# Performance work log

Measured on AMD Instinct MI355X. Metric: run time of the kernel, lower is better.

Reference implementation:

```python
import math
import jax, jax.numpy as jnp
import numpy as np

C = 256
CQ = C // 8
B, H, W = 8, 64, 64


def setup_inputs() -> dict:
    key = jax.random.key(0)
    k1, k2, k3, k4 = jax.random.split(key, 4)
    x = jax.random.normal(k1, (B, C, H, W), dtype=jnp.float32)
    # 1x1 conv weights, bias=False -> plain [out, in] matrices
    wq = jax.random.normal(k2, (CQ, C), dtype=jnp.float32) * 0.02
    wk = jax.random.normal(k3, (CQ, C), dtype=jnp.float32) * 0.02
    wv = jax.random.normal(k4, (C, C), dtype=jnp.float32) * 0.02
    # gamma init is zeros in the torch module; use small nonzero so output depends on attention path
    gamma = jnp.ones((1,), dtype=jnp.float32) * 0.5
    return {"x": x, "wq": wq, "wk": wk, "wv": wv, "gamma": gamma}


def reference(x, wq, wk, wv, gamma):
    b, c, h, w = x.shape
    n = h * w
    xr = x.reshape(b, c, n)                       # [B, C, N]
    q = jnp.einsum('oc,bcn->bon', wq, xr)         # [B, Cq, N]
    k = jnp.einsum('oc,bcn->bon', wk, xr)         # [B, Cq, N]
    v = jnp.einsum('oc,bcn->bon', wv, xr)         # [B, C, N]
    # attn[b, i, j] = softmax_j( q[:, i] . k[:, j] / sqrt(Cq) )
    scores = jnp.einsum('bci,bcj->bij', q, k) / math.sqrt(q.shape[1])  # [B, N, N]
    attn = jax.nn.softmax(scores, axis=-1)
    # out[b, c, m] = sum_n v[b, c, n] * attn[b, m, n]
    out = jnp.einsum('bcn,bmn->bcm', v, attn).reshape(b, c, h, w)
    return gamma[0] * out + x
```

## Files before the change

### kernel.cpp

```cpp
#include <hip/hip_runtime.h>

#define B_ 8
#define C_ 256
#define CQ_ 32
#define N_ 4096

typedef __attribute__((ext_vector_type(8))) short short8;
typedef __attribute__((ext_vector_type(4))) float float4v;

#define QSCALE 0.2550599232f

#if __has_builtin(__builtin_amdgcn_exp2f)
#define EXP2F __builtin_amdgcn_exp2f
#else
#define EXP2F exp2f
#endif

static __device__ __forceinline__ unsigned short f2bf(float f) {
  unsigned int u = __float_as_uint(f);
  u += 0x7FFFu + ((u >> 16) & 1u);
  return (unsigned short)(u >> 16);
}

static __device__ __forceinline__ void async16(void* lds, const void* g) {
  __builtin_amdgcn_global_load_lds(
      (const __attribute__((address_space(1))) unsigned int*)g,
      (__attribute__((address_space(3))) unsigned int*)lds, 16, 0, 0);
}

__global__ __launch_bounds__(256) void conv_kernel(
    const float* __restrict__ x, const float* __restrict__ wq,
    const float* __restrict__ wk, const float* __restrict__ wv,
    unsigned short* __restrict__ xT, unsigned short* __restrict__ w_bf) {
  int tid = threadIdx.x, nt = blockIdx.x, b = blockIdx.y;
  if (nt == 64) {
    #pragma unroll 1
    for (int i = 0; i < 40; ++i) {
      int o = b * 40 + i;
      const float* src; float sc = 1.f;
      if (o < 32)      { src = wq + (size_t)o * 256; sc = QSCALE; }
      else if (o < 64) { src = wk + (size_t)(o - 32) * 256; }
      else             { src = wv + (size_t)(o - 64) * 256; }
      w_bf[o * 256 + tid] = f2bf(src[tid] * sc);
    }
    return;
  }
  __shared__ __align__(16) unsigned short t_lds[16 * 264];
  int n0 = nt * 64;
  const float* xp = x + ((size_t)b * C_ + tid) * N_ + n0;
  #pragma unroll 1
  for (int nl = 0; nl < 4; ++nl) {
    float4 f[4];
    #pragma unroll
    for (int i = 0; i < 4; ++i) f[i] = *(const float4*)(xp + nl * 16 + i * 4);
    if (nl) __syncthreads();
    #pragma unroll
    for (int i = 0; i < 4; ++i) {
      t_lds[(i * 4 + 0) * 264 + tid] = f2bf(f[i].x);
      t_lds[(i * 4 + 1) * 264 + tid] = f2bf(f[i].y);
      t_lds[(i * 4 + 2) * 264 + tid] = f2bf(f[i].z);
      t_lds[(i * 4 + 3) * 264 + tid] = f2bf(f[i].w);
    }
    __syncthreads();
    int row = tid >> 4, col = (tid & 15) * 16;
    uint4 a0 = *(const uint4*)(&t_lds[row * 264 + col]);
    uint4 a1 = *(const uint4*)(&t_lds[row * 264 + col + 8]);
    unsigned short* dst = xT + ((size_t)b * N_ + n0 + nl * 16 + row) * 256 + col;
    *(uint4*)(dst) = a0;
    *(uint4*)(dst + 8) = a1;
  }
}

__global__ __launch_bounds__(256, 2) void proj_kernel(
    const unsigned short* __restrict__ xT, const unsigned short* __restrict__ w_bf,
    unsigned short* __restrict__ qT, unsigned short* __restrict__ kT,
    unsigned short* __restrict__ v) {
  __shared__ __align__(16) unsigned short xb[2][256 * 32];
  int tid = threadIdx.x, wave = tid >> 6, lane = tid & 63;
  int q16 = lane >> 4, l16 = lane & 15;
  int b = blockIdx.x, n0 = blockIdx.y * 256, ot = blockIdx.z;

  short8 af[4][8];
  #pragma unroll
  for (int mt = 0; mt < 4; ++mt)
    #pragma unroll
    for (int ks = 0; ks < 8; ++ks)
      af[mt][ks] = *(const short8*)(w_bf + (size_t)(ot * 64 + mt * 16 + l16) * 256 + ks * 32 + q16 * 8);

  const unsigned short* xbase = xT + ((size_t)b * N_ + n0) * 256;
  auto stage = [&](int buf, int ks) {
    #pragma unroll
    for (int it = 0; it < 4; ++it) {
      int r = wave * 64 + it * 16 + (lane >> 2);
      int lo = (lane & 3) ^ ((r >> 1) & 3);
      async16(&xb[buf][(wave * 64 + it * 16) * 32],
              xbase + (size_t)r * 256 + ks * 32 + lo * 8);
    }
  };

  float4v acc[4][4];
  float4v zerov = {0.f, 0.f, 0.f, 0.f};
  #pragma unroll
  for (int mt = 0; mt < 4; ++mt)
    for (int nt = 0; nt < 4; ++nt) acc[mt][nt] = zerov;

  stage(0, 0);
  __syncthreads();

  int po = (( l16 >> 1) & 3);
  #pragma unroll
  for (int ks = 0; ks < 8; ++ks) {
    if (ks < 7) stage((ks + 1) & 1, ks + 1);
    short8 bf4[4];
    #pragma unroll
    for (int nt = 0; nt < 4; ++nt) {
      int row = wave * 64 + nt * 16 + l16;
      bf4[nt] = *(const short8*)(&xb[ks & 1][row * 32 + (q16 ^ po) * 8]);
    }
    #pragma unroll
    for (int mt = 0; mt < 4; ++mt)
      #pragma unroll
      for (int nt = 0; nt < 4; ++nt)
        acc[mt][nt] = __builtin_amdgcn_mfma_f32_16x16x32_bf16(af[mt][ks], bf4[nt], acc[mt][nt], 0, 0, 0);
    __syncthreads();
  }

  #pragma unroll
  for (int mt = 0; mt < 4; ++mt) {
    int og0 = ot * 64 + mt * 16;
    #pragma unroll
    for (int nt = 0; nt < 4; ++nt) {
      int n = n0 + wave * 64 + nt * 16 + l16;
      if (og0 < 64) {
        unsigned short* dst = (og0 < 32) ? qT : kT;
        int obase = og0 & 31;
        unsigned short t[4];
        #pragma unroll
        for (int r = 0; r < 4; ++r) t[r] = f2bf(acc[mt][nt][r]);
        *(uint2*)(dst + ((size_t)b * N_ + n) * CQ_ + obase + q16 * 4) = *(const uint2*)t;
      } else {
        int c0 = og0 - 64 + q16 * 4;
        #pragma unroll
        for (int r = 0; r < 4; ++r)
          v[((size_t)b * C_ + c0 + r) * N_ + n] = f2bf(acc[mt][nt][r]);
      }
    }
  }
}

__global__ __launch_bounds__(256, 3) void attn_kernel(
    const unsigned short* __restrict__ qT, const unsigned short* __restrict__ kT,
    const unsigned short* __restrict__ v, const float* __restrict__ x,
    const float* __restrict__ gamma, float* __restrict__ out) {
  __shared__ __align__(16) unsigned short v_lds[256 * 64];
  __shared__ __align__(16) unsigned short kt_lds[2][64 * 32];
  __shared__ __align__(16) unsigned short p_lds[64 * 64];
  __shared__ float l_lds[64];

  int tid = threadIdx.x, wave = tid >> 6, lane = tid & 63;
  int q16 = lane >> 4, l16 = lane & 15;
  int bid = blockIdx.x, b = bid & 7, m0 = (bid >> 3) * 64;

  short8 qfrag = *(const short8*)(qT + ((size_t)b * N_ + m0 + wave * 16 + l16) * CQ_ + q16 * 8);

  const unsigned short* vbase = v + (size_t)b * C_ * N_;
  auto stageV = [&](int j0) {
    #pragma unroll
    for (int it = 0; it < 8; ++it) {
      int r = wave * 64 + it * 8 + (lane >> 3);
      int lo = (lane & 7) ^ (lane >> 3);
      async16(&v_lds[(wave * 64 + it * 8) * 64], vbase + (size_t)r * N_ + j0 + lo * 8);
    }
  };
  auto stageK = [&](int buf, int j0) {
    int r = wave * 16 + (lane >> 2);
    int lo = (lane & 3) ^ ((r >> 1) & 3);
    async16(&kt_lds[buf][wave * 16 * 32], kT + ((size_t)b * N_ + j0 + r) * CQ_ + lo * 8);
  };

  stageK(0, 0);
  stageV(0);
  __syncthreads();

  float4v acc[4][4];
  float4v zerov = {0.f, 0.f, 0.f, 0.f};
  #pragma unroll
  for (int mt = 0; mt < 4; ++mt)
    for (int ct = 0; ct < 4; ++ct) acc[mt][ct] = zerov;
  float lrun[4] = {0.f, 0.f, 0.f, 0.f};

  int kro = q16 ^ ((l16 >> 1) & 3);
  int vro = l16 & 7;
  int lo8 = l16 >> 3, li = l16 & 7;

  for (int j = 0; j < 64; ++j) {
    const unsigned short* ktb = kt_lds[j & 1];
    float4v s[4];
    #pragma unroll
    for (int jt = 0; jt < 4; ++jt) {
      short8 kf = *(const short8*)(&ktb[(jt * 16 + l16) * 32 + kro * 8]);
      s[jt] = __builtin_amdgcn_mfma_f32_16x16x32_bf16(qfrag, kf, zerov, 0, 0, 0);
    }
    #pragma unroll
    for (int r = 0; r < 4; ++r) {
      float p0 = EXP2F(s[0][r]), p1 = EXP2F(s[1][r]);
      float p2 = EXP2F(s[2][r]), p3 = EXP2F(s[3][r]);
      lrun[r] += (p0 + p1) + (p2 + p3);
      int prow = wave * 16 + q16 * 4 + r;
      int rl = (q16 * 4 + r) & 7;
      unsigned short* pr = &p_lds[prow * 64 + li];
      int o0 = lo8 ^ rl;
      pr[(o0 ^ 0) * 8] = (unsigned short)(__float_as_uint(p0) >> 16);
      pr[(o0 ^ 2) * 8] = (unsigned short)(__float_as_uint(p1) >> 16);
      pr[(o0 ^ 4) * 8] = (unsigned short)(__float_as_uint(p2) >> 16);
      pr[(o0 ^ 6) * 8] = (unsigned short)(__float_as_uint(p3) >> 16);
    }
    if (j == 63) {
      #pragma unroll
      for (int r = 0; r < 4; ++r) {
        float t = lrun[r];
        t += __shfl_xor(t, 1); t += __shfl_xor(t, 2);
        t += __shfl_xor(t, 4); t += __shfl_xor(t, 8);
        if (l16 == 0) l_lds[wave * 16 + q16 * 4 + r] = t;
      }
    }
    __syncthreads();

    if (j < 63) stageK((j + 1) & 1, (j + 1) * 64);

    #pragma unroll
    for (int ks = 0; ks < 2; ++ks) {
      short8 pf[4], vf[4];
      #pragma unroll
      for (int mt = 0; mt < 4; ++mt)
        pf[mt] = *(const short8*)(&p_lds[(mt * 16 + l16) * 64 + (((ks * 4 + q16) ^ vro) * 8)]);
      #pragma unroll
      for (int ct = 0; ct < 4; ++ct)
        vf[ct] = *(const short8*)(&v_lds[(wave * 64 + ct * 16 + l16) * 64 + (((ks * 4 + q16) ^ vro) * 8)]);
      #pragma unroll
      for (int mt = 0; mt < 4; ++mt)
        #pragma unroll
        for (int ct = 0; ct < 4; ++ct)
          acc[mt][ct] = __builtin_amdgcn_mfma_f32_16x16x32_bf16(pf[mt], vf[ct], acc[mt][ct], 0, 0, 0);
    }
    __syncthreads();

    if (j < 63) stageV((j + 1) * 64);
  }

  float g = gamma[0];
  #pragma unroll
  for (int mt = 0; mt < 4; ++mt) {
    float linv[4];
    #pragma unroll
    for (int r = 0; r < 4; ++r) linv[r] = 1.f / l_lds[mt * 16 + q16 * 4 + r];
    int n = m0 + mt * 16 + q16 * 4;
    #pragma unroll
    for (int ct = 0; ct < 4; ++ct) {
      int c = wave * 64 + ct * 16 + l16;
      size_t off = ((size_t)b * C_ + c) * N_ + n;
      float4 xv = *(const float4*)(x + off);
      float4 o;
      o.x = g * acc[mt][ct][0] * linv[0] + xv.x;
      o.y = g * acc[mt][ct][1] * linv[1] + xv.y;
      o.z = g * acc[mt][ct][2] * linv[2] + xv.z;
      o.w = g * acc[mt][ct][3] * linv[3] + xv.w;
      *(float4*)(out + off) = o;
    }
  }
}

extern "C" void kernel_launch(void* const* d_in, const int* in_sizes, int n_in,
                              void* d_out, int out_size, void* d_ws, size_t ws_size,
                              hipStream_t stream) {
  const float* x     = (const float*)d_in[0];
  const float* wq    = (const float*)d_in[1];
  const float* wk    = (const float*)d_in[2];
  const float* wv    = (const float*)d_in[3];
  const float* gamma = (const float*)d_in[4];
  float* out = (float*)d_out;

  unsigned short* qT  = (unsigned short*)d_ws;
  unsigned short* kT  = qT + (size_t)B_ * N_ * CQ_;
  unsigned short* vv  = kT + (size_t)B_ * N_ * CQ_;
  unsigned short* xT  = vv + (size_t)B_ * C_ * N_;
  unsigned short* wbf = xT + (size_t)B_ * N_ * C_;

  hipLaunchKernelGGL(conv_kernel, dim3(65, 8), dim3(256), 0, stream,
                     x, wq, wk, wv, xT, wbf);
  hipLaunchKernelGGL(proj_kernel, dim3(8, 16, 5), dim3(256), 0, stream,
                     xT, wbf, qT, kT, vv);
  hipLaunchKernelGGL(attn_kernel, dim3(512), dim3(256), 0, stream,
                     qT, kT, vv, x, gamma, out);
}
```

Baseline: 206.5 us.

## Fuse x transpose into projection and stream V into registers in attention

The separate x-to-bf16 transpose kernel is removed. The projection kernel now reads fp32 x directly, converts it, and writes swizzled bf16 tiles into LDS; each block computes all 320 output channels for 64 pixels, with weights loaded from global memory per k-step. In attention, V is no longer staged in LDS. Each wave loads its V fragments from global memory straight into double-buffered registers, P is double-buffered in LDS, and one barrier per iteration is removed. The aim is to cut the extra xT round trip through global memory, LDS traffic and barriers, at the cost of more registers (occupancy hint lowered to 2) and exposed global-load latency for V.

```diff
diff --git a/kernel.cpp b/kernel.cpp
--- a/kernel.cpp
+++ b/kernel.cpp
@@ -28,133 +28,106 @@
       (__attribute__((address_space(3))) unsigned int*)lds, 16, 0, 0);
 }
 
-__global__ __launch_bounds__(256) void conv_kernel(
-    const float* __restrict__ x, const float* __restrict__ wq,
-    const float* __restrict__ wk, const float* __restrict__ wv,
-    unsigned short* __restrict__ xT, unsigned short* __restrict__ w_bf) {
-  int tid = threadIdx.x, nt = blockIdx.x, b = blockIdx.y;
-  if (nt == 64) {
-    #pragma unroll 1
-    for (int i = 0; i < 40; ++i) {
-      int o = b * 40 + i;
-      const float* src; float sc = 1.f;
-      if (o < 32)      { src = wq + (size_t)o * 256; sc = QSCALE; }
-      else if (o < 64) { src = wk + (size_t)(o - 32) * 256; }
-      else             { src = wv + (size_t)(o - 64) * 256; }
-      w_bf[o * 256 + tid] = f2bf(src[tid] * sc);
-    }
-    return;
-  }
-  __shared__ __align__(16) unsigned short t_lds[16 * 264];
-  int n0 = nt * 64;
-  const float* xp = x + ((size_t)b * C_ + tid) * N_ + n0;
-  #pragma unroll 1
-  for (int nl = 0; nl < 4; ++nl) {
-    float4 f[4];
-    #pragma unroll
-    for (int i = 0; i < 4; ++i) f[i] = *(const float4*)(xp + nl * 16 + i * 4);
-    if (nl) __syncthreads();
-    #pragma unroll
-    for (int i = 0; i < 4; ++i) {
-      t_lds[(i * 4 + 0) * 264 + tid] = f2bf(f[i].x);
-      t_lds[(i * 4 + 1) * 264 + tid] = f2bf(f[i].y);
-      t_lds[(i * 4 + 2) * 264 + tid] = f2bf(f[i].z);
-      t_lds[(i * 4 + 3) * 264 + tid] = f2bf(f[i].w);
-    }
-    __syncthreads();
-    int row = tid >> 4, col = (tid & 15) * 16;
-    uint4 a0 = *(const uint4*)(&t_lds[row * 264 + col]);
-    uint4 a1 = *(const uint4*)(&t_lds[row * 264 + col + 8]);
-    unsigned short* dst = xT + ((size_t)b * N_ + n0 + nl * 16 + row) * 256 + col;
-    *(uint4*)(dst) = a0;
-    *(uint4*)(dst + 8) = a1;
-  }
+__global__ __launch_bounds__(256) void wconv_kernel(
+    const float* __restrict__ wq, const float* __restrict__ wk,
+    const float* __restrict__ wv, unsigned short* __restrict__ w_bf) {
+  int o = blockIdx.x * 8 + (threadIdx.x >> 5);
+  int c8 = (threadIdx.x & 31) * 8;
+  const float* src; float sc = 1.f;
+  if (o < 32)      { src = wq + (size_t)o * 256; sc = QSCALE; }
+  else if (o < 64) { src = wk + (size_t)(o - 32) * 256; }
+  else             { src = wv + (size_t)(o - 64) * 256; }
+  float4 a = *(const float4*)(src + c8);
+  float4 bq = *(const float4*)(src + c8 + 4);
+  unsigned short t[8] = {f2bf(a.x*sc), f2bf(a.y*sc), f2bf(a.z*sc), f2bf(a.w*sc),
+                         f2bf(bq.x*sc), f2bf(bq.y*sc), f2bf(bq.z*sc), f2bf(bq.w*sc)};
+  *(uint4*)(w_bf + (size_t)o * 256 + c8) = *(const uint4*)t;
 }
 
 __global__ __launch_bounds__(256, 2) void proj_kernel(
-    const unsigned short* __restrict__ xT, const unsigned short* __restrict__ w_bf,
+    const float* __restrict__ x, const unsigned short* __restrict__ w_bf,
     unsigned short* __restrict__ qT, unsigned short* __restrict__ kT,
     unsigned short* __restrict__ v) {
-  __shared__ __align__(16) unsigned short xb[2][256 * 32];
+  __shared__ __align__(16) unsigned short xb[2][64 * 32];
   int tid = threadIdx.x, wave = tid >> 6, lane = tid & 63;
   int q16 = lane >> 4, l16 = lane & 15;
-  int b = blockIdx.x, n0 = blockIdx.y * 256, ot = blockIdx.z;
-
-  short8 af[4][8];
-  #pragma unroll
-  for (int mt = 0; mt < 4; ++mt)
-    #pragma unroll
-    for (int ks = 0; ks < 8; ++ks)
-      af[mt][ks] = *(const short8*)(w_bf + (size_t)(ot * 64 + mt * 16 + l16) * 256 + ks * 32 + q16 * 8);
-
-  const unsigned short* xbase = xT + ((size_t)b * N_ + n0) * 256;
+  int b = blockIdx.x, n0 = blockIdx.y * 64;
+
+  int p = tid & 15, n4g = tid >> 4;
+  const float* x0 = x + (size_t)b * C_ * N_ + n0 + n4g * 4;
+
   auto stage = [&](int buf, int ks) {
-    #pragma unroll
-    for (int it = 0; it < 4; ++it) {
-      int r = wave * 64 + it * 16 + (lane >> 2);
-      int lo = (lane & 3) ^ ((r >> 1) & 3);
-      async16(&xb[buf][(wave * 64 + it * 16) * 32],
-              xbase + (size_t)r * 256 + ks * 32 + lo * 8);
+    const float* r0 = x0 + (size_t)(ks * 32 + 2 * p) * N_;
+    float4 fa = *(const float4*)(r0);
+    float4 fb = *(const float4*)(r0 + N_);
+    float va[4] = {fa.x, fa.y, fa.z, fa.w};
+    float vb[4] = {fb.x, fb.y, fb.z, fb.w};
+    #pragma unroll
+    for (int i = 0; i < 4; ++i) {
+      int n = n4g * 4 + i;
+      unsigned int pk = (unsigned int)f2bf(va[i]) | ((unsigned int)f2bf(vb[i]) << 16);
+      int so = (p >> 2) ^ ((n >> 1) & 3);
+      *(unsigned int*)(&xb[buf][n * 32 + so * 8 + (p & 3) * 2]) = pk;
     }
   };
 
-  float4v acc[4][4];
+  float4v acc[5][4];
   float4v zerov = {0.f, 0.f, 0.f, 0.f};
   #pragma unroll
-  for (int mt = 0; mt < 4; ++mt)
+  for (int mt = 0; mt < 5; ++mt)
     for (int nt = 0; nt < 4; ++nt) acc[mt][nt] = zerov;
 
   stage(0, 0);
   __syncthreads();
 
-  int po = (( l16 >> 1) & 3);
-  #pragma unroll
+  int o0 = wave * 80;
+  int sxo = (q16 ^ ((l16 >> 1) & 3)) * 8;
+  #pragma unroll 1
   for (int ks = 0; ks < 8; ++ks) {
     if (ks < 7) stage((ks + 1) & 1, ks + 1);
-    short8 bf4[4];
+    short8 af[5], bf4[4];
+    #pragma unroll
+    for (int mt = 0; mt < 5; ++mt)
+      af[mt] = *(const short8*)(w_bf + (size_t)(o0 + mt * 16 + l16) * 256 + ks * 32 + q16 * 8);
+    #pragma unroll
+    for (int nt = 0; nt < 4; ++nt)
+      bf4[nt] = *(const short8*)(&xb[ks & 1][(nt * 16 + l16) * 32 + sxo]);
+    #pragma unroll
+    for (int mt = 0; mt < 5; ++mt)
+      #pragma unroll
+      for (int nt = 0; nt < 4; ++nt)
+        acc[mt][nt] = __builtin_amdgcn_mfma_f32_16x16x32_bf16(af[mt], bf4[nt], acc[mt][nt], 0, 0, 0);
+    __syncthreads();
+  }
+
+  #pragma unroll
+  for (int mt = 0; mt < 5; ++mt) {
+    int og = o0 + mt * 16 + q16 * 4;
     #pragma unroll
     for (int nt = 0; nt < 4; ++nt) {
-      int row = wave * 64 + nt * 16 + l16;
-      bf4[nt] = *(const short8*)(&xb[ks & 1][row * 32 + (q16 ^ po) * 8]);
-    }
-    #pragma unroll
-    for (int mt = 0; mt < 4; ++mt)
-      #pragma unroll
-      for (int nt = 0; nt < 4; ++nt)
-        acc[mt][nt] = __builtin_amdgcn_mfma_f32_16x16x32_bf16(af[mt][ks], bf4[nt], acc[mt][nt], 0, 0, 0);
-    __syncthreads();
-  }
-
-  #pragma unroll
-  for (int mt = 0; mt < 4; ++mt) {
-    int og0 = ot * 64 + mt * 16;
-    #pragma unroll
-    for (int nt = 0; nt < 4; ++nt) {
-      int n = n0 + wave * 64 + nt * 16 + l16;
-      if (og0 < 64) {
-        unsigned short* dst = (og0 < 32) ? qT : kT;
-        int obase = og0 & 31;
-        unsigned short t[4];
+      int n = n0 + nt * 16 + l16;
+      unsigned short t[4];
+      if (og < 64) {
         #pragma unroll
         for (int r = 0; r < 4; ++r) t[r] = f2bf(acc[mt][nt][r]);
-        *(uint2*)(dst + ((size_t)b * N_ + n) * CQ_ + obase + q16 * 4) = *(const uint2*)t;
+        unsigned short* dst = (og < 32) ? (qT + ((size_t)b * N_ + n) * CQ_ + og)
+                                        : (kT + ((size_t)b * N_ + n) * CQ_ + (og - 32));
+        *(uint2*)dst = *(const uint2*)t;
       } else {
-        int c0 = og0 - 64 + q16 * 4;
         #pragma unroll
         for (int r = 0; r < 4; ++r)
-          v[((size_t)b * C_ + c0 + r) * N_ + n] = f2bf(acc[mt][nt][r]);
+          v[((size_t)b * C_ + og - 64 + r) * N_ + n] = f2bf(acc[mt][nt][r]);
       }
     }
   }
 }
 
-__global__ __launch_bounds__(256, 3) void attn_kernel(
+__global__ __launch_bounds__(256, 2) void attn_kernel(
     const unsigned short* __restrict__ qT, const unsigned short* __restrict__ kT,
     const unsigned short* __restrict__ v, const float* __restrict__ x,
     const float* __restrict__ gamma, float* __restrict__ out) {
-  __shared__ __align__(16) unsigned short v_lds[256 * 64];
   __shared__ __align__(16) unsigned short kt_lds[2][64 * 32];
-  __shared__ __align__(16) unsigned short p_lds[64 * 64];
+  __shared__ __align__(16) unsigned short p_lds[2][64 * 64];
   __shared__ float l_lds[64];
 
   int tid = threadIdx.x, wave = tid >> 6, lane = tid & 63;
@@ -163,24 +136,26 @@
 
   short8 qfrag = *(const short8*)(qT + ((size_t)b * N_ + m0 + wave * 16 + l16) * CQ_ + q16 * 8);
 
-  const unsigned short* vbase = v + (size_t)b * C_ * N_;
-  auto stageV = [&](int j0) {
-    #pragma unroll
-    for (int it = 0; it < 8; ++it) {
-      int r = wave * 64 + it * 8 + (lane >> 3);
-      int lo = (lane & 7) ^ (lane >> 3);
-      async16(&v_lds[(wave * 64 + it * 8) * 64], vbase + (size_t)r * N_ + j0 + lo * 8);
-    }
-  };
   auto stageK = [&](int buf, int j0) {
     int r = wave * 16 + (lane >> 2);
     int lo = (lane & 3) ^ ((r >> 1) & 3);
     async16(&kt_lds[buf][wave * 16 * 32], kT + ((size_t)b * N_ + j0 + r) * CQ_ + lo * 8);
   };
 
+  const unsigned short* vw = v + ((size_t)b * C_ + wave * 64) * N_;
+  uint4 vfr[2][8];
+  auto vload = [&](uint4* dst, int j0) {
+    #pragma unroll
+    for (int ks = 0; ks < 2; ++ks)
+      #pragma unroll
+      for (int ct = 0; ct < 4; ++ct)
+        dst[ks * 4 + ct] =
+            *(const uint4*)(vw + (size_t)(ct * 16 + l16) * N_ + j0 + ks * 32 + q16 * 8);
+  };
+
   stageK(0, 0);
-  stageV(0);
   __syncthreads();
+  vload(vfr[0], 0);
 
   float4v acc[4][4];
   float4v zerov = {0.f, 0.f, 0.f, 0.f};
@@ -193,14 +168,17 @@
   int vro = l16 & 7;
   int lo8 = l16 >> 3, li = l16 & 7;
 
+  #pragma unroll 2
   for (int j = 0; j < 64; ++j) {
-    const unsigned short* ktb = kt_lds[j & 1];
+    int cur = j & 1;
     float4v s[4];
     #pragma unroll
     for (int jt = 0; jt < 4; ++jt) {
-      short8 kf = *(const short8*)(&ktb[(jt * 16 + l16) * 32 + kro * 8]);
+      short8 kf = *(const short8*)(&kt_lds[cur][(jt * 16 + l16) * 32 + kro * 8]);
       s[jt] = __builtin_amdgcn_mfma_f32_16x16x32_bf16(qfrag, kf, zerov, 0, 0, 0);
     }
+    if (j < 63) stageK(cur ^ 1, (j + 1) * 64);
+
     #pragma unroll
     for (int r = 0; r < 4; ++r) {
       float p0 = EXP2F(s[0][r]), p1 = EXP2F(s[1][r]);
@@ -208,7 +186,7 @@
       lrun[r] += (p0 + p1) + (p2 + p3);
       int prow = wave * 16 + q16 * 4 + r;
       int rl = (q16 * 4 + r) & 7;
-      unsigned short* pr = &p_lds[prow * 64 + li];
+      unsigned short* pr = &p_lds[cur][prow * 64 + li];
       int o0 = lo8 ^ rl;
       pr[(o0 ^ 0) * 8] = (unsigned short)(__float_as_uint(p0) >> 16);
       pr[(o0 ^ 2) * 8] = (unsigned short)(__float_as_uint(p1) >> 16);
@@ -226,26 +204,22 @@
     }
     __syncthreads();
 
-    if (j < 63) stageK((j + 1) & 1, (j + 1) * 64);
+    if (j < 63) vload(vfr[cur ^ 1], (j + 1) * 64);
 
     #pragma unroll
     for (int ks = 0; ks < 2; ++ks) {
-      short8 pf[4], vf[4];
+      short8 pf[4];
       #pragma unroll
       for (int mt = 0; mt < 4; ++mt)
-        pf[mt] = *(const short8*)(&p_lds[(mt * 16 + l16) * 64 + (((ks * 4 + q16) ^ vro) * 8)]);
-      #pragma unroll
-      for (int ct = 0; ct < 4; ++ct)
-        vf[ct] = *(const short8*)(&v_lds[(wave * 64 + ct * 16 + l16) * 64 + (((ks * 4 + q16) ^ vro) * 8)]);
-      #pragma unroll
-      for (int mt = 0; mt < 4; ++mt)
+        pf[mt] = *(const short8*)(&p_lds[cur][(mt * 16 + l16) * 64 + ((ks * 4 + q16) ^ vro) * 8]);
+      #pragma unroll
+      for (int ct = 0; ct < 4; ++ct) {
+        short8 vf = *(const short8*)&vfr[cur][ks * 4 + ct];
         #pragma unroll
-        for (int ct = 0; ct < 4; ++ct)
-          acc[mt][ct] = __builtin_amdgcn_mfma_f32_16x16x32_bf16(pf[mt], vf[ct], acc[mt][ct], 0, 0, 0);
-    }
-    __syncthreads();
-
-    if (j < 63) stageV((j + 1) * 64);
+        for (int mt = 0; mt < 4; ++mt)
+          acc[mt][ct] = __builtin_amdgcn_mfma_f32_16x16x32_bf16(pf[mt], vf, acc[mt][ct], 0, 0, 0);
+      }
+    }
   }
 
   float g = gamma[0];
@@ -283,13 +257,9 @@
   unsigned short* qT  = (unsigned short*)d_ws;
   unsigned short* kT  = qT + (size_t)B_ * N_ * CQ_;
   unsigned short* vv  = kT + (size_t)B_ * N_ * CQ_;
-  unsigned short* xT  = vv + (size_t)B_ * C_ * N_;
-  unsigned short* wbf = xT + (size_t)B_ * N_ * C_;
-
-  hipLaunchKernelGGL(conv_kernel, dim3(65, 8), dim3(256), 0, stream,
-                     x, wq, wk, wv, xT, wbf);
-  hipLaunchKernelGGL(proj_kernel, dim3(8, 16, 5), dim3(256), 0, stream,
-                     xT, wbf, qT, kT, vv);
-  hipLaunchKernelGGL(attn_kernel, dim3(512), dim3(256), 0, stream,
-                     qT, kT, vv, x, gamma, out);
-}
+  unsigned short* wbf = vv + (size_t)B_ * C_ * N_;
+
+  hipLaunchKernelGGL(wconv_kernel, dim3(40), dim3(256), 0, stream, wq, wk, wv, wbf);
+  hipLaunchKernelGGL(proj_kernel, dim3(8, 64), dim3(256), 0, stream, x, wbf, qT, kT, vv);
+  hipLaunchKernelGGL(attn_kernel, dim3(512), dim3(256), 0, stream, qT, kT, vv, x, gamma, out);
+}
```

Result: slower. 228.6 us (+10.7%).
